# Performance work log

Hardware: AMD Instinct MI355X
Metric: run time of the kernel (lower is better)

## Reference

```python
import jax, jax.numpy as jnp
import numpy as np

MAX_SEQ, D, VOCAB, N_LAYERS = 2048, 256, 240, 6
DH = 64.0  # scale used inside RelativeGlobalAttention
BATCH = 4


def _pos_embedding():
    # sin(pow(pos*1e-5, i/D) - pi/2 * ((i+1)%2)), exactly as in __init__
    pos = np.arange(MAX_SEQ, dtype=np.float64)[:, None]
    i = np.arange(D, dtype=np.float64)[None, :]
    ang = np.power(pos * 1e-5, i / D) - np.pi * 0.5 * ((i + 1) % 2)
    return jnp.asarray(np.sin(ang), dtype=jnp.float32)  # [L, D]


def _skew(QE):
    # pad a zero column in front, reshape [B,L,L+1]->[B,L+1,L], drop first row
    B, L, _ = QE.shape
    cat = jnp.concatenate([jnp.zeros((B, L, 1), QE.dtype), QE], axis=2)
    return cat.reshape(B, L + 1, L)[:, 1:, :]


def _rel_attn(x, Wq, Wk, Wv):
    Q = x @ Wq  # [B,L,D]
    K = x @ Wk
    V = x @ Wv
    QE = jnp.einsum('bld,bmd->blm', Q, K - Q)      # Q @ (K-Q)^T
    Srel = _skew(QE)
    QKt = jnp.einsum('bld,bmd->blm', Q, K)
    scores = (QKt + Srel) / jnp.sqrt(jnp.asarray(DH, x.dtype))
    probs = jax.nn.softmax(scores, axis=-1)        # no causal mask in source
    return probs @ V


def setup_inputs() -> dict:
    key = jax.random.key(0)
    ks = jax.random.split(key, 16)
    s = 1.0 / np.sqrt(D)
    mk = lambda k, shape, sc: (jax.random.normal(k, shape, jnp.float32) * sc)
    inp = {
        'tokens': jax.random.randint(ks[0], (BATCH, MAX_SEQ), 0, VOCAB),
        'embed_table': mk(ks[1], (VOCAB, D), 0.05),
        'Wq1': mk(ks[2], (N_LAYERS, D, D), s),
        'Wk1': mk(ks[3], (N_LAYERS, D, D), s),
        'Wv1': mk(ks[4], (N_LAYERS, D, D), s),
        'Wq2': mk(ks[5], (N_LAYERS, D, D), s),
        'Wk2': mk(ks[6], (N_LAYERS, D, D), s),
        'Wv2': mk(ks[7], (N_LAYERS, D, D), s),
        'Wf1': mk(ks[8], (N_LAYERS, D, D), s),
        'bf1': jnp.zeros((N_LAYERS, D), jnp.float32),
        'Wf2': mk(ks[9], (N_LAYERS, D, D), s),
        'bf2': jnp.zeros((N_LAYERS, D), jnp.float32),
        'Wfc': mk(ks[10], (MAX_SEQ * D, VOCAB), 1.0 / np.sqrt(MAX_SEQ * D)),
        'bfc': jnp.zeros((VOCAB,), jnp.float32),
    }
    return inp


def reference(tokens, embed_table, Wq1, Wk1, Wv1, Wq2, Wk2, Wv2,
              Wf1, bf1, Wf2, bf2, Wfc, bfc):
    x = embed_table[tokens] + _pos_embedding()[None]  # [B,L,D]
    for i in range(N_LAYERS):
        x = _rel_attn(x, Wq1[i], Wk1[i], Wv1[i]) + x
        x = _rel_attn(x, Wq2[i], Wk2[i], Wv2[i]) + x
        h = jax.nn.leaky_relu(x @ Wf1[i] + bf1[i], negative_slope=0.2)
        x = h @ Wf2[i] + bf2[i]
        # NOTE: BatchNorm layers exist in source but are never called in _decoder
    flat = x.reshape(x.shape[0], -1)  # [B, L*D]
    return jax.nn.softmax(flat @ Wfc + bfc, axis=-1)  # [B, vocab]
```

## Files before the change

### kernel.cpp

```cpp
#include <hip/hip_runtime.h>
#include <hip/hip_fp16.h>

typedef unsigned short u16;
typedef unsigned int   u32;

#define BB 4
#define LL 2048
#define DD 256
#define VV 240
#define NLAYERS 6

static constexpr long BLD = (long)BB * LL * DD;
static constexpr long LD_ = (long)LL * DD;
static constexpr long LxL = (long)LL * LL;
static constexpr long BLL = (long)BB * LxL;

typedef _Float16 h8  __attribute__((ext_vector_type(8)));
typedef float  f32x4 __attribute__((ext_vector_type(4)));

__device__ __forceinline__ u16 f2h(float f) {
    _Float16 h = (_Float16)f;
    return __builtin_bit_cast(u16, h);
}
__device__ __forceinline__ float h2f(u16 u) {
    return (float)__builtin_bit_cast(_Float16, u);
}

__device__ __forceinline__ void gl16(const void* g, void* l) {
    __builtin_amdgcn_global_load_lds((const __attribute__((address_space(1))) void*)g,
                                     (__attribute__((address_space(3))) void*)l, 16, 0, 0);
}

__device__ __forceinline__ uint3 swz_bid() {
    const int gx = gridDim.x, gy = gridDim.y;
    const int nwg = gx * gy * gridDim.z;
    const int lin = blockIdx.x + gx * (blockIdx.y + gy * blockIdx.z);
    const int q = nwg >> 3;
    const int swz = (lin & 7) * q + (lin >> 3);
    uint3 r;
    r.x = swz % gx;
    const int t2 = swz / gx;
    r.y = t2 % gy;
    r.z = t2 / gy;
    return r;
}

__global__ __launch_bounds__(256)
void embed_kernel(const int* __restrict__ tokens, const float* __restrict__ table,
                  float* __restrict__ x, u16* __restrict__ xh)
{
    long idx = (long)blockIdx.x * 256 + threadIdx.x;
    if (idx >= BLD) return;
    int i  = (int)(idx & (DD - 1));
    long bl = idx >> 8;
    int l  = (int)(bl & (LL - 1));
    int tok = tokens[bl];
    float base = (float)l * 1e-5f;
    float p = powf(base, (float)i * (1.0f / (float)DD));
    float ang = p - ((i & 1) ? 0.0f : 1.57079632679489662f);
    float v = table[(long)tok * DD + i] + sinf(ang);
    x[idx] = v;
    xh[idx] = f2h(v);
}

template<bool DIFF>
__global__ __launch_bounds__(256)
void wconv(const float* __restrict__ W, const float* __restrict__ Wsub,
           u16* __restrict__ Wt, long lstride)
{
    int blk = blockIdx.x;
    int m  = blk >> 6;
    int ti = (blk >> 3) & 7;
    int tj = blk & 7;
    const float* src = W + (long)m * 65536;
    u16* dst = Wt + (long)m * lstride;
    __shared__ float tile[32][33];
    int t = threadIdx.x;
    int c = t & 31, r8 = t >> 5;
    #pragma unroll
    for (int p = 0; p < 4; ++p) {
        int r = r8 + p * 8;
        long off = (long)(ti * 32 + r) * 256 + tj * 32 + c;
        float v = src[off];
        if constexpr (DIFF) v -= Wsub[(long)m * 65536 + off];
        tile[r][c] = v;
    }
    __syncthreads();
    #pragma unroll
    for (int p = 0; p < 4; ++p) {
        int n = r8 + p * 8;
        dst[(long)(tj * 32 + n) * 256 + ti * 32 + c] = f2h(tile[c][n]);
    }
}

template<int EPI, int BM, int BN>
__global__ __launch_bounds__(256)
void gemm_mfma(const u16* __restrict__ A, const u16* __restrict__ B,
               const u16* __restrict__ B2,
               const float* __restrict__ bias, const float* __restrict__ Cres,
               float* __restrict__ Cf, u16* __restrict__ Ch,
               u16* __restrict__ Ch2, u16* __restrict__ Ch3, u16* __restrict__ Ch4,
               int M, int N, int K, int ldA,
               long sA, long sB, long sC)
{
    constexpr int FM = BM / 32, FN = BN / 32;
    __shared__ u16 As[2][BM * 32];
    __shared__ u16 Bs[2][BN * 32];
    const uint3 bid = swz_bid();
    const int bz = bid.z;
    A += (long)bz * sA;
    const int bm = bid.y * BM;
    const int bn = bid.x * BN;
    int bnb = bn;
    const u16* Bp;
    if constexpr (EPI & 128) {
        Bp = (bn >= LL) ? B2 : B;
        if (bn >= LL) bnb = bn - LL;
        Bp += (long)bz * sB;
    } else {
        Bp = B + (long)bz * sB;
    }
    if constexpr (EPI & 4)  Cres += (long)bz * sC;
    if constexpr (EPI & 8)  Cf   += (long)bz * sC;
    if constexpr ((EPI & 16) && !(EPI & (64 | 128))) Ch += (long)bz * sC;

    const int t = threadIdx.x;
    const int lane = t & 63, wave = t >> 6;
    const int wm = (wave >> 1) * (BM / 2), wn = (wave & 1) * (BN / 2);

    f32x4 acc[FM][FN];
    #pragma unroll
    for (int i = 0; i < FM; ++i)
        #pragma unroll
        for (int j = 0; j < FN; ++j)
            acc[i][j] = (f32x4){0.f, 0.f, 0.f, 0.f};

    const u16* gA0 = A  + (long)(bm  + (t >> 2)) * ldA + (t & 3) * 8;
    const u16* gB0 = Bp + (long)(bnb + (t >> 2)) * K   + (t & 3) * 8;

    const int arow = wm + (lane & 15);
    const int brow = wn + (lane & 15);
    const int ko = (lane >> 4) * 8;

    #define STAGE(buf, koff) do {                                              \
        gl16(gA0 + (koff), &As[buf][wave * 512]);                              \
        if constexpr (BM == 128) gl16(gA0 + 64L * ldA + (koff),                \
                                      &As[buf][2048 + wave * 512]);            \
        gl16(gB0 + (koff), &Bs[buf][wave * 512]);                              \
        if constexpr (BN == 128) gl16(gB0 + 64L * K + (koff),                  \
                                      &Bs[buf][2048 + wave * 512]);            \
    } while (0)

    STAGE(0, 0);
    int cur = 0;
    for (int k0 = 0; k0 < K; k0 += 32) {
        __syncthreads();
        if (k0 + 32 < K) {
            if (cur) STAGE(0, k0 + 32);
            else     STAGE(1, k0 + 32);
        }
        h8 af[FM], bf[FN];
        #pragma unroll
        for (int i = 0; i < FM; ++i) af[i] = *(const h8*)&As[cur][(arow + i * 16) * 32 + ko];
        #pragma unroll
        for (int j = 0; j < FN; ++j) bf[j] = *(const h8*)&Bs[cur][(brow + j * 16) * 32 + ko];
        #pragma unroll
        for (int i = 0; i < FM; ++i)
            #pragma unroll
            for (int j = 0; j < FN; ++j)
                acc[i][j] = __builtin_amdgcn_mfma_f32_16x16x32_f16(af[i], bf[j], acc[i][j], 0, 0, 0);
        cur ^= 1;
    }
    #undef STAGE

    const int colc = lane & 15;
    const int rowb = (lane >> 4) * 4;
    if constexpr (EPI & 64) {
        const int seg = bn >> 8;
        const int nb  = bn & 255;
        if (seg < 3) {
            u16* dst = (seg == 0) ? Ch : ((seg == 1) ? Ch2 : Ch3);
            #pragma unroll
            for (int i = 0; i < FM; ++i)
                #pragma unroll
                for (int j = 0; j < FN; ++j) {
                    int nn = nb + wn + j * 16 + colc;
                    #pragma unroll
                    for (int r = 0; r < 4; ++r) {
                        long row = bm + wm + i * 16 + rowb + r;
                        dst[row * DD + nn] = f2h(acc[i][j][r]);
                    }
                }
        } else {
            #pragma unroll
            for (int i = 0; i < FM; ++i) {
                int r0 = bm + wm + i * 16 + rowb;
                int b  = r0 >> 11;
                int m0 = r0 & (LL - 1);
                #pragma unroll
                for (int j = 0; j < FN; ++j) {
                    int nn = nb + wn + j * 16 + colc;
                    f32x4 v = acc[i][j];
                    ushort4 pk;
                    pk.x = f2h(v.x); pk.y = f2h(v.y); pk.z = f2h(v.z); pk.w = f2h(v.w);
                    *(ushort4*)&Ch4[((long)b * DD + nn) * LL + m0] = pk;
                }
            }
        }
    } else if constexpr (EPI & 128) {
        u16* dst = ((bn >= LL) ? Ch2 : Ch) + (long)bz * sC;
        const int nb = bn & (LL - 1);
        #pragma unroll
        for (int i = 0; i < FM; ++i)
            #pragma unroll
            for (int j = 0; j < FN; ++j) {
                int n = nb + wn + j * 16 + colc;
                #pragma unroll
                for (int r = 0; r < 4; ++r) {
                    long row = bm + wm + i * 16 + rowb + r;
                    dst[row * LL + n] = f2h(acc[i][j][r]);
                }
            }
    } else {
        #pragma unroll
        for (int i = 0; i < FM; ++i) {
            #pragma unroll
            for (int j = 0; j < FN; ++j) {
                int n = bn + wn + j * 16 + colc;
                float bv = (EPI & 1) ? bias[n] : 0.f;
                #pragma unroll
                for (int r = 0; r < 4; ++r) {
                    long row = bm + wm + i * 16 + rowb + r;
                    float val = acc[i][j][r] + bv;
                    if (EPI & 2) val = (val >= 0.f) ? val : 0.2f * val;
                    long off = row * (long)N + n;
                    if (EPI & 4) val += Cres[off];
                    if (EPI & 8) Cf[off] = val;
                    if (EPI & 16) Ch[off] = f2h(val);
                }
            }
        }
    }
}

__global__ __launch_bounds__(256)
void skew_softmax(u16* __restrict__ S1, const u16* __restrict__ QE)
{
    const int bi = blockIdx.x;
    const int b = bi >> 11;
    const int i = bi & (LL - 1);
    u16* srow = S1 + (long)bi * LL;
    const u16* qe_i  = QE + ((long)b * LL + i) * LL;
    const u16* qe_i1 = qe_i + ((i + 1 < LL) ? LL : 0);
    const int t = threadIdx.x;

    uint4 sv = ((const uint4*)srow)[t];
    const u16* se = (const u16*)&sv;
    float vals[8];
    float mx = -1e30f;
    #pragma unroll
    for (int j = 0; j < 8; ++j) {
        int m = t * 8 + j;
        float srel;
        if (m <= i)            srel = h2f(qe_i[m - i + (LL - 1)]);
        else if (m == i + 1)   srel = 0.f;
        else                   srel = h2f(qe_i1[m - i - 2]);
        float s = (h2f(se[j]) + srel) * 0.125f;
        vals[j] = s;
        mx = fmaxf(mx, s);
    }
    #pragma unroll
    for (int off = 32; off >= 1; off >>= 1)
        mx = fmaxf(mx, __shfl_xor(mx, off, 64));
    __shared__ float redm[4], reds[4];
    const int wid = t >> 6;
    if ((t & 63) == 0) redm[wid] = mx;
    __syncthreads();
    mx = fmaxf(fmaxf(redm[0], redm[1]), fmaxf(redm[2], redm[3]));

    float sum = 0.f;
    #pragma unroll
    for (int j = 0; j < 8; ++j) { vals[j] = expf(vals[j] - mx); sum += vals[j]; }
    #pragma unroll
    for (int off = 32; off >= 1; off >>= 1)
        sum += __shfl_xor(sum, off, 64);
    if ((t & 63) == 0) reds[wid] = sum;
    __syncthreads();
    sum = reds[0] + reds[1] + reds[2] + reds[3];
    float inv = 1.0f / sum;
    uint4 ov;
    u16* oe = (u16*)&ov;
    #pragma unroll
    for (int j = 0; j < 8; ++j) oe[j] = f2h(vals[j] * inv);
    ((uint4*)srow)[t] = ov;
}

__global__ __launch_bounds__(960)
void fc_partial(const float* __restrict__ x, const float* __restrict__ W,
                float* __restrict__ part)
{
    const int v = threadIdx.x;
    const int b = threadIdx.y;
    const int chunk = blockIdx.x;
    const int KC = (int)(LD_ / 256);
    const long k0 = (long)chunk * KC;
    const float* xb = x + (long)b * LD_ + k0;
    const float* Wp = W + k0 * VV + v;
    float acc = 0.f;
    #pragma unroll 4
    for (int k2 = 0; k2 < KC; ++k2)
        acc = fmaf(xb[k2], Wp[(long)k2 * VV], acc);
    part[((long)chunk * BB + b) * VV + v] = acc;
}

__global__ __launch_bounds__(960)
void fc_finish(const float* __restrict__ part, const float* __restrict__ bias,
               float* __restrict__ out)
{
    const int v = threadIdx.x, b = threadIdx.y;
    float acc = bias[v];
    for (int c = 0; c < 256; ++c)
        acc += part[((long)c * BB + b) * VV + v];
    __shared__ float lds[BB][VV];
    __shared__ float mxs[BB], sms[BB];
    lds[b][v] = acc;
    __syncthreads();
    if (v == 0) {
        float m = -1e30f;
        for (int j = 0; j < VV; ++j) m = fmaxf(m, lds[b][j]);
        float s = 0.f;
        for (int j = 0; j < VV; ++j) s += expf(lds[b][j] - m);
        mxs[b] = m; sms[b] = s;
    }
    __syncthreads();
    out[b * VV + v] = expf(lds[b][v] - mxs[b]) / sms[b];
}

extern "C" void kernel_launch(void* const* d_in, const int* in_sizes, int n_in,
                              void* d_out, int out_size, void* d_ws, size_t ws_size,
                              hipStream_t stream)
{
    const int*   tokens = (const int*)d_in[0];
    const float* table  = (const float*)d_in[1];
    const float* Wq1 = (const float*)d_in[2];
    const float* Wk1 = (const float*)d_in[3];
    const float* Wv1 = (const float*)d_in[4];
    const float* Wq2 = (const float*)d_in[5];
    const float* Wk2 = (const float*)d_in[6];
    const float* Wv2 = (const float*)d_in[7];
    const float* Wf1 = (const float*)d_in[8];
    const float* bf1 = (const float*)d_in[9];
    const float* Wf2 = (const float*)d_in[10];
    const float* bf2 = (const float*)d_in[11];
    const float* Wfc = (const float*)d_in[12];
    const float* bfc = (const float*)d_in[13];

    char* p = (char*)d_ws;
    float* x  = (float*)p; p += BLD * 4;
    u16* xh = (u16*)p;     p += BLD * 2;
    u16* qb = (u16*)p;     p += BLD * 2;
    u16* kb = (u16*)p;     p += BLD * 2;
    u16* eb = (u16*)p;     p += BLD * 2;
    u16* vt = (u16*)p;     p += BLD * 2;
    u16* S1 = (u16*)p;     p += BLL * 2;
    u16* QE = (u16*)p;     p += BLL * 2;
    u16* qkevw = (u16*)p;  p += 12L * 4 * 65536 * 2;
    u16* fw = (u16*)p;     p += 12L * 65536 * 2;
    float* part = (float*)p;
    u16* hb = qb;

    const long LS = 4 * 65536;
    wconv<false><<<384, 256, 0, stream>>>(Wq1, nullptr, qkevw + 0L * 65536, LS);
    wconv<false><<<384, 256, 0, stream>>>(Wk1, nullptr, qkevw + 1L * 65536, LS);
    wconv<true ><<<384, 256, 0, stream>>>(Wk1, Wq1,     qkevw + 2L * 65536, LS);
    wconv<false><<<384, 256, 0, stream>>>(Wv1, nullptr, qkevw + 3L * 65536, LS);
    wconv<false><<<384, 256, 0, stream>>>(Wq2, nullptr, qkevw + 24L * 65536, LS);
    wconv<true ><<<384, 256, 0, stream>>>(Wk2, Wq2,     qkevw + 24L * 65536 + 2 * 65536, LS);
    wconv<false><<<384, 256, 0, stream>>>(Wk2, nullptr, qkevw + 24L * 65536 + 1 * 65536, LS);
    wconv<false><<<384, 256, 0, stream>>>(Wv2, nullptr, qkevw + 24L * 65536 + 3 * 65536, LS);
    wconv<false><<<384, 256, 0, stream>>>(Wf1, nullptr, fw, 65536);
    wconv<false><<<384, 256, 0, stream>>>(Wf2, nullptr, fw + 6L * 65536, 65536);

    embed_kernel<<<(int)((BLD + 255) / 256), 256, 0, stream>>>(tokens, table, x, xh);

    const dim3 gqkev(8, 64, 1);
    const dim3 gscore(32, 16, BB);
    const dim3 gpv(4, 16, BB);
    const dim3 gffn(4, 64, 1);

    for (int layer = 0; layer < NLAYERS; ++layer) {
        for (int half = 0; half < 2; ++half) {
            const u16* wqkev = qkevw + ((long)(half * 6 + layer)) * LS;
            gemm_mfma<64, 128, 128><<<gqkev, 256, 0, stream>>>(
                xh, wqkev, nullptr, nullptr, nullptr, nullptr, qb, kb, eb, vt,
                BB * LL, 1024, DD, DD, 0, 0, 0);
            gemm_mfma<128, 128, 128><<<gscore, 256, 0, stream>>>(
                qb, kb, eb, nullptr, nullptr, nullptr, S1, QE, nullptr, nullptr,
                LL, LL, DD, DD, LD_, LD_, LxL);
            skew_softmax<<<BB * LL, 256, 0, stream>>>(S1, QE);
            gemm_mfma<4 | 8 | 16, 128, 64><<<gpv, 256, 0, stream>>>(
                S1, vt, nullptr, nullptr, x, x, xh, nullptr, nullptr, nullptr,
                LL, DD, LL, LL, LxL, LD_, LD_);
        }
        gemm_mfma<1 | 2 | 16, 128, 64><<<gffn, 256, 0, stream>>>(
            xh, fw + (long)layer * 65536, nullptr, bf1 + layer * DD, nullptr,
            nullptr, hb, nullptr, nullptr, nullptr, BB * LL, DD, DD, DD, 0, 0, 0);
        gemm_mfma<1 | 8 | 16, 128, 64><<<gffn, 256, 0, stream>>>(
            hb, fw + (long)(6 + layer) * 65536, nullptr, bf2 + layer * DD, nullptr,
            x, xh, nullptr, nullptr, nullptr, BB * LL, DD, DD, DD, 0, 0, 0);
    }

    fc_partial<<<256, dim3(VV, BB, 1), 0, stream>>>(x, Wfc, part);
    fc_finish<<<1, dim3(VV, BB, 1), 0, stream>>>(part, bfc, (float*)d_out);
}
```

Before: 1.665 ms.

## Batch weight conversions into one launch, precompute positional table, retile PV/FFN GEMMs

Merges the ten separate weight-conversion launches into a single kernel that reads its parameters from a struct array, cutting launch overhead. The positional embedding is computed once per (l,i) into a table instead of per batch element, which removes repeated powf/sinf work. The PV and FFN GEMMs change tile shape from 128x64 to 64x128, with the grids adjusted to match. This alters how many blocks run and how the N dimension is covered. The tile change is the only part that touches the main loop and carries most of the risk of a regression.

```diff
diff --git a/kernel.cpp b/kernel.cpp
--- a/kernel.cpp
+++ b/kernel.cpp
@@ -46,7 +46,20 @@
 }
 
 __global__ __launch_bounds__(256)
+void pe_kernel(float* __restrict__ pe)
+{
+    int idx = blockIdx.x * 256 + threadIdx.x;
+    int i = idx & (DD - 1);
+    int l = idx >> 8;
+    float base = (float)l * 1e-5f;
+    float p = powf(base, (float)i * (1.0f / (float)DD));
+    float ang = p - ((i & 1) ? 0.0f : 1.57079632679489662f);
+    pe[idx] = sinf(ang);
+}
+
+__global__ __launch_bounds__(256)
 void embed_kernel(const int* __restrict__ tokens, const float* __restrict__ table,
+                  const float* __restrict__ pe,
                   float* __restrict__ x, u16* __restrict__ xh)
 {
     long idx = (long)blockIdx.x * 256 + threadIdx.x;
@@ -55,25 +68,30 @@
     long bl = idx >> 8;
     int l  = (int)(bl & (LL - 1));
     int tok = tokens[bl];
-    float base = (float)l * 1e-5f;
-    float p = powf(base, (float)i * (1.0f / (float)DD));
-    float ang = p - ((i & 1) ? 0.0f : 1.57079632679489662f);
-    float v = table[(long)tok * DD + i] + sinf(ang);
+    float v = table[(long)tok * DD + i] + pe[(long)l * DD + i];
     x[idx] = v;
     xh[idx] = f2h(v);
 }
 
-template<bool DIFF>
+struct WcArgs {
+    const float* src[10];
+    const float* sub[10];
+    u16*         dst[10];
+    long         lstride[10];
+};
+
 __global__ __launch_bounds__(256)
-void wconv(const float* __restrict__ W, const float* __restrict__ Wsub,
-           u16* __restrict__ Wt, long lstride)
+void wconv_all(WcArgs a)
 {
     int blk = blockIdx.x;
-    int m  = blk >> 6;
-    int ti = (blk >> 3) & 7;
-    int tj = blk & 7;
-    const float* src = W + (long)m * 65536;
-    u16* dst = Wt + (long)m * lstride;
+    int which = blk / 384;
+    int rest  = blk % 384;
+    int m  = rest >> 6;
+    int ti = (rest >> 3) & 7;
+    int tj = rest & 7;
+    const float* src = a.src[which] + (long)m * 65536;
+    const float* sub = a.sub[which];
+    u16* dst = a.dst[which] + (long)m * a.lstride[which];
     __shared__ float tile[32][33];
     int t = threadIdx.x;
     int c = t & 31, r8 = t >> 5;
@@ -82,7 +100,7 @@
         int r = r8 + p * 8;
         long off = (long)(ti * 32 + r) * 256 + tj * 32 + c;
         float v = src[off];
-        if constexpr (DIFF) v -= Wsub[(long)m * 65536 + off];
+        if (sub) v -= sub[(long)m * 65536 + off];
         tile[r][c] = v;
     }
     __syncthreads();
@@ -366,27 +384,31 @@
     u16* QE = (u16*)p;     p += BLL * 2;
     u16* qkevw = (u16*)p;  p += 12L * 4 * 65536 * 2;
     u16* fw = (u16*)p;     p += 12L * 65536 * 2;
+    float* pe = (float*)p; p += LD_ * 4;
     float* part = (float*)p;
     u16* hb = qb;
 
     const long LS = 4 * 65536;
-    wconv<false><<<384, 256, 0, stream>>>(Wq1, nullptr, qkevw + 0L * 65536, LS);
-    wconv<false><<<384, 256, 0, stream>>>(Wk1, nullptr, qkevw + 1L * 65536, LS);
-    wconv<true ><<<384, 256, 0, stream>>>(Wk1, Wq1,     qkevw + 2L * 65536, LS);
-    wconv<false><<<384, 256, 0, stream>>>(Wv1, nullptr, qkevw + 3L * 65536, LS);
-    wconv<false><<<384, 256, 0, stream>>>(Wq2, nullptr, qkevw + 24L * 65536, LS);
-    wconv<true ><<<384, 256, 0, stream>>>(Wk2, Wq2,     qkevw + 24L * 65536 + 2 * 65536, LS);
-    wconv<false><<<384, 256, 0, stream>>>(Wk2, nullptr, qkevw + 24L * 65536 + 1 * 65536, LS);
-    wconv<false><<<384, 256, 0, stream>>>(Wv2, nullptr, qkevw + 24L * 65536 + 3 * 65536, LS);
-    wconv<false><<<384, 256, 0, stream>>>(Wf1, nullptr, fw, 65536);
-    wconv<false><<<384, 256, 0, stream>>>(Wf2, nullptr, fw + 6L * 65536, 65536);
-
-    embed_kernel<<<(int)((BLD + 255) / 256), 256, 0, stream>>>(tokens, table, x, xh);
+    WcArgs wa;
+    wa.src[0] = Wq1; wa.sub[0] = nullptr; wa.dst[0] = qkevw + 0L * 65536;  wa.lstride[0] = LS;
+    wa.src[1] = Wk1; wa.sub[1] = nullptr; wa.dst[1] = qkevw + 1L * 65536;  wa.lstride[1] = LS;
+    wa.src[2] = Wk1; wa.sub[2] = Wq1;     wa.dst[2] = qkevw + 2L * 65536;  wa.lstride[2] = LS;
+    wa.src[3] = Wv1; wa.sub[3] = nullptr; wa.dst[3] = qkevw + 3L * 65536;  wa.lstride[3] = LS;
+    wa.src[4] = Wq2; wa.sub[4] = nullptr; wa.dst[4] = qkevw + 24L * 65536; wa.lstride[4] = LS;
+    wa.src[5] = Wk2; wa.sub[5] = nullptr; wa.dst[5] = qkevw + 24L * 65536 + 1 * 65536; wa.lstride[5] = LS;
+    wa.src[6] = Wk2; wa.sub[6] = Wq2;     wa.dst[6] = qkevw + 24L * 65536 + 2 * 65536; wa.lstride[6] = LS;
+    wa.src[7] = Wv2; wa.sub[7] = nullptr; wa.dst[7] = qkevw + 24L * 65536 + 3 * 65536; wa.lstride[7] = LS;
+    wa.src[8] = Wf1; wa.sub[8] = nullptr; wa.dst[8] = fw;                  wa.lstride[8] = 65536;
+    wa.src[9] = Wf2; wa.sub[9] = nullptr; wa.dst[9] = fw + 6L * 65536;     wa.lstride[9] = 65536;
+    wconv_all<<<3840, 256, 0, stream>>>(wa);
+
+    pe_kernel<<<(int)(LD_ / 256), 256, 0, stream>>>(pe);
+    embed_kernel<<<(int)((BLD + 255) / 256), 256, 0, stream>>>(tokens, table, pe, x, xh);
 
     const dim3 gqkev(8, 64, 1);
     const dim3 gscore(32, 16, BB);
-    const dim3 gpv(4, 16, BB);
-    const dim3 gffn(4, 64, 1);
+    const dim3 gpv(2, 32, BB);
+    const dim3 gffn(2, 128, 1);
 
     for (int layer = 0; layer < NLAYERS; ++layer) {
         for (int half = 0; half < 2; ++half) {
@@ -398,14 +420,14 @@
                 qb, kb, eb, nullptr, nullptr, nullptr, S1, QE, nullptr, nullptr,
                 LL, LL, DD, DD, LD_, LD_, LxL);
             skew_softmax<<<BB * LL, 256, 0, stream>>>(S1, QE);
-            gemm_mfma<4 | 8 | 16, 128, 64><<<gpv, 256, 0, stream>>>(
+            gemm_mfma<4 | 8 | 16, 64, 128><<<gpv, 256, 0, stream>>>(
                 S1, vt, nullptr, nullptr, x, x, xh, nullptr, nullptr, nullptr,
                 LL, DD, LL, LL, LxL, LD_, LD_);
         }
-        gemm_mfma<1 | 2 | 16, 128, 64><<<gffn, 256, 0, stream>>>(
+        gemm_mfma<1 | 2 | 16, 64, 128><<<gffn, 256, 0, stream>>>(
             xh, fw + (long)layer * 65536, nullptr, bf1 + layer * DD, nullptr,
             nullptr, hb, nullptr, nullptr, nullptr, BB * LL, DD, DD, DD, 0, 0, 0);
-        gemm_mfma<1 | 8 | 16, 128, 64><<<gffn, 256, 0, stream>>>(
+        gemm_mfma<1 | 8 | 16, 64, 128><<<gffn, 256, 0, stream>>>(
             hb, fw + (long)(6 + layer) * 65536, nullptr, bf2 + layer * DD, nullptr,
             x, xh, nullptr, nullptr, nullptr, BB * LL, DD, DD, DD, 0, 0, 0);
     }
```

Result: no change. 1.658 ms (-0.4%).
